# Performance work log

Measured on AMD Instinct MI355X. Metric: run time of the kernel, lower is better.

Reference implementation:

```python
import jax, jax.numpy as jnp
import numpy as np

EPS = 1e-12  # F.normalize eps
WIN_SIZE = 200
WIN_STEP = 30  # eval mode (training uses 10)
N_WIN = 30     # 31 windows from length-1100 axis, last one dropped


def setup_inputs() -> dict:
    key = jax.random.key(0)
    ks = jax.random.split(key, 6)
    dim, K, out_dim = 128, 64, 256
    N, H, W = 8, 16, 900
    s = 1.0 / np.sqrt(dim)
    return {
        "x": jax.random.normal(ks[0], (N, dim, H, W), dtype=jnp.float32),
        "cluster_centers": jax.random.uniform(ks[1], (K, dim), dtype=jnp.float32),
        "conv_w": jax.random.normal(ks[2], (K, dim), dtype=jnp.float32) * s,
        "conv_b": jax.random.normal(ks[3], (K,), dtype=jnp.float32) * s,
        "mlp_w": jax.random.normal(ks[4], (out_dim, K * dim), dtype=jnp.float32) * s,
        "mlp_b": jax.random.normal(ks[5], (out_dim,), dtype=jnp.float32) * s,
    }


def _l2norm(v, axis):
    return v / jnp.clip(jnp.linalg.norm(v, axis=axis, keepdims=True), EPS)


def reference(x, cluster_centers, conv_w, conv_b, mlp_w, mlp_b):
    N, C, H, W = x.shape
    K = conv_w.shape[0]
    # 1x1 conv -> soft assignment, softmax over clusters (dim=1 after view(N,K,HW))
    logits = jnp.einsum('nchw,kc->nkhw', x, conv_w) + conv_b[None, :, None, None]
    a = jax.nn.softmax(logits, axis=1)  # (N,K,H,W)
    # Fused weighted residual sum over H (torch sums dim=-2 of (N,K,C,H,W)):
    # vlad_pre[n,k,c,w] = sum_h a[n,k,h,w]*x[n,c,h,w] - centers[k,c]*sum_h a[n,k,h,w]
    wx = jnp.einsum('nkhw,nchw->nkcw', a, x)               # (N,K,C,W)
    asum = a.sum(axis=2)                                    # (N,K,W)
    res = wx - cluster_centers[None, :, :, None] * asum[:, :, None, :]
    # circular pad along yaw: [800:] ++ all ++ [:100] -> length 1100
    res = jnp.concatenate([res[..., 800:], res, res[..., :100]], axis=-1)
    # sliding-window sum, size 200 step 30, drop last window -> 30 windows
    cs = jnp.cumsum(res, axis=-1)
    cs = jnp.concatenate([jnp.zeros(res.shape[:-1] + (1,), res.dtype), cs], axis=-1)
    starts = jnp.arange(N_WIN) * WIN_STEP
    win = cs[..., starts + WIN_SIZE] - cs[..., starts]      # (N,K,C,30)
    vlad = jnp.transpose(win, (0, 3, 1, 2)).reshape(N * N_WIN, K, C)
    vlad = _l2norm(vlad, axis=2)                            # intra-norm per cluster
    vlad = _l2norm(vlad.reshape(N * N_WIN, K * C), axis=1)  # global norm
    out = vlad @ mlp_w.T + mlp_b
    out = _l2norm(out, axis=1)
    return out.reshape(N, N_WIN, -1)
```

## Files before the change

kernel.cpp:

```cpp
#include <hip/hip_runtime.h>
#include <cstddef>

#define EPSF 1e-12f
#define NCB 90
#define NT 30
#define ODIM 256
#define DDIM 8192

typedef unsigned short u16;
typedef __attribute__((ext_vector_type(8))) short short8;
typedef __attribute__((ext_vector_type(4))) float float4v;

__device__ inline u16 f2bf(float f) {
  union { float f; unsigned u; } v; v.f = f;
  unsigned r = v.u + 0x7FFFu + ((v.u >> 16) & 1u);
  return (u16)(r >> 16);
}
__device__ inline float bf2f(u16 h) {
  union { unsigned u; float f; } v; v.u = ((unsigned)h) << 16;
  return v.f;
}

__global__ __launch_bounds__(256, 2) void k1_assign(
    const float* __restrict__ x,
    const float* __restrict__ conv_w,
    const float* __restrict__ conv_b,
    float* __restrict__ P,
    float* __restrict__ PA)
{
  __shared__ u16 wfh[8192];
  __shared__ u16 wfl[8192];
  __shared__ u16 xtf[4096];
  __shared__ u16 xf[4096];
  __shared__ float As[64 * 33];
  __shared__ u16 afr[2048];
  __shared__ float Mf[32];
  __shared__ float sm4[128];
  __shared__ float pasum[256];

  const int bx = blockIdx.x;
  const int n = bx / NCB, cb = bx - n * NCB;
  const int t = threadIdx.x;
  const int lane = t & 63;
  const int w = t >> 6;

  const float* xn = x + (size_t)n * 1843200 + cb * 10;

#pragma unroll 4
  for (int i = 0; i < 32; ++i) {
    int e = t + 256 * i;
    int k = e >> 7, c = e & 127;
    float wv = conv_w[e];
    u16 h = f2bf(wv);
    float lo = wv - bf2f(h);
    int idx = (((k >> 4) * 4 + (c >> 5)) * 64 + (((c >> 3) & 3) << 4) + (k & 15)) * 8 + (c & 7);
    wfh[idx] = h;
    wfl[idx] = f2bf(lo);
  }

  const int colt = w & 1;
  const int kt0 = w >> 1;
  const float bk0 = conv_b[kt0 * 16 + (lane & 15)];
  const float bk1 = conv_b[(kt0 + 2) * 16 + (lane & 15)];

  float4v pacc[8];
#pragma unroll
  for (int i = 0; i < 8; ++i) pacc[i] = (float4v){0.f, 0.f, 0.f, 0.f};
  float pak = 0.f;

  for (int cc = 0; cc < 5; ++cc) {
    __syncthreads();
#pragma unroll
    for (int s = 0; s < 8; ++s) {
      int e2 = t + 256 * s;
      int c = e2 >> 4, p = e2 & 15;
      int cl = 2 * p;
      int g = cc * 32 + cl;
      int h = g / 10, wi = g - 10 * h;
      float2 val = *(const float2*)(xn + (size_t)c * 14400 + h * 900 + wi);
      u16 h0 = f2bf(val.x), h1 = f2bf(val.y);
      int ip = ((c >> 4) * 64 + ((cl >> 3) << 4) + (c & 15)) * 8 + (cl & 7);
      ushort2 pr; pr.x = h0; pr.y = h1;
      *(ushort2*)&xf[ip] = pr;
      int base_t = (((cl >> 4) * 4 + (c >> 5)) * 64 + (((c >> 3) & 3) << 4)) * 8 + (c & 7);
      xtf[base_t + ((cl & 15) << 3)] = h0;
      xtf[base_t + (((cl + 1) & 15) << 3)] = h1;
    }
    __syncthreads();

    {
      float4v d0 = (float4v){0.f, 0.f, 0.f, 0.f};
      float4v d1 = (float4v){0.f, 0.f, 0.f, 0.f};
#pragma unroll
      for (int cb32 = 0; cb32 < 4; ++cb32) {
        short8 xa = *(short8*)&xtf[((colt * 4 + cb32) * 64 + lane) * 8];
        short8 w0h = *(short8*)&wfh[((kt0 * 4 + cb32) * 64 + lane) * 8];
        short8 w0l = *(short8*)&wfl[((kt0 * 4 + cb32) * 64 + lane) * 8];
        short8 w1h = *(short8*)&wfh[(((kt0 + 2) * 4 + cb32) * 64 + lane) * 8];
        short8 w1l = *(short8*)&wfl[(((kt0 + 2) * 4 + cb32) * 64 + lane) * 8];
        d0 = __builtin_amdgcn_mfma_f32_16x16x32_bf16(xa, w0h, d0, 0, 0, 0);
        d0 = __builtin_amdgcn_mfma_f32_16x16x32_bf16(xa, w0l, d0, 0, 0, 0);
        d1 = __builtin_amdgcn_mfma_f32_16x16x32_bf16(xa, w1h, d1, 0, 0, 0);
        d1 = __builtin_amdgcn_mfma_f32_16x16x32_bf16(xa, w1l, d1, 0, 0, 0);
      }
      int colb = colt * 16 + ((lane >> 4) << 2);
      int kr0 = kt0 * 16 + (lane & 15);
      int kr1 = (kt0 + 2) * 16 + (lane & 15);
#pragma unroll
      for (int r = 0; r < 4; ++r) {
        As[kr0 * 33 + colb + r] = d0[r] + bk0;
        As[kr1 * 33 + colb + r] = d1[r] + bk1;
      }
    }
    __syncthreads();

    if (t < 32) {
      float m = -3.4e38f;
#pragma unroll
      for (int kk = 0; kk < 64; ++kk) m = fmaxf(m, As[kk * 33 + t]);
      Mf[t] = m;
    }
    __syncthreads();
    if (t < 128) {
      int col = t & 31, kg = t >> 5;
      float M = Mf[col], s = 0.f;
#pragma unroll
      for (int ii = 0; ii < 16; ++ii) {
        int a = (kg * 16 + ii) * 33 + col;
        float e = __expf(As[a] - M);
        As[a] = e;
        s += e;
      }
      sm4[kg * 32 + col] = s;
    }
    __syncthreads();

    {
      int k = t & 63, cg = t >> 6;
      union { u16 u[8]; short8 v; } cvt;
      float paks = 0.f;
#pragma unroll
      for (int j = 0; j < 8; ++j) {
        int col = cg * 8 + j;
        float inv = 1.f / (sm4[col] + sm4[32 + col] + sm4[64 + col] + sm4[96 + col]);
        float a = As[k * 33 + col] * inv;
        paks += a;
        cvt.u[j] = f2bf(a);
      }
      pak += paks;
      int dst = ((k >> 4) * 64 + (cg << 4) + (k & 15)) * 8;
      *(short8*)&afr[dst] = cvt.v;
    }
    __syncthreads();

    {
      short8 aa = *(short8*)&afr[(w * 64 + lane) * 8];
#pragma unroll
      for (int ct = 0; ct < 8; ++ct) {
        short8 xb = *(short8*)&xf[(ct * 64 + lane) * 8];
        pacc[ct] = __builtin_amdgcn_mfma_f32_16x16x32_bf16(aa, xb, pacc[ct], 0, 0, 0);
      }
    }
  }

  float* Pp = P + (size_t)(n * NCB + cb) * DDIM;
  {
    int krow = w * 16 + ((lane >> 4) << 2);
    int c0 = lane & 15;
#pragma unroll
    for (int ct = 0; ct < 8; ++ct)
#pragma unroll
      for (int r = 0; r < 4; ++r)
        Pp[(krow + r) * 128 + ct * 16 + c0] = pacc[ct][r];
  }
  pasum[t] = pak;
  __syncthreads();
  if (t < 64)
    PA[(size_t)(n * NCB + cb) * 64 + t] =
        pasum[t] + pasum[64 + t] + pasum[128 + t] + pasum[192 + t];
}

__global__ __launch_bounds__(256) void k2_vlad(
    const float* __restrict__ P, const float* __restrict__ PA,
    const float* __restrict__ centers, float* __restrict__ vlad,
    float* __restrict__ gss)
{
  __shared__ float Ak[16];
  __shared__ float red[4];
  const int b = blockIdx.x;
  const int win = b >> 2, eb = b & 3;
  const int n = win / NT, wt = win - n * NT;
  const int t = threadIdx.x;

  if (t < 64) {
    int kk = t >> 2, ii = t & 3;
    float s = 0.f;
#pragma unroll
    for (int ss = 0; ss < 5; ++ss) {
      int i = ii + 4 * ss;
      int cb = (3 * wt + 80 + i) % 90;
      s += PA[((size_t)n * NCB + cb) * 64 + eb * 16 + kk];
    }
    s += __shfl_xor(s, 1);
    s += __shfl_xor(s, 2);
    if (ii == 0) Ak[kk] = s;
  }
  __syncthreads();

  const int e0 = eb * 2048 + t * 8;
  float v[8];
#pragma unroll
  for (int j = 0; j < 8; ++j) v[j] = 0.f;
#pragma unroll 5
  for (int i = 0; i < 20; ++i) {
    int cb = (3 * wt + 80 + i) % 90;
    const float* Pp = P + ((size_t)n * NCB + cb) * DDIM + e0;
    float4 u0 = *(const float4*)Pp;
    float4 u1 = *(const float4*)(Pp + 4);
    v[0] += u0.x; v[1] += u0.y; v[2] += u0.z; v[3] += u0.w;
    v[4] += u1.x; v[5] += u1.y; v[6] += u1.z; v[7] += u1.w;
  }
  const float A = Ak[t >> 4];
  const float* ce = centers + e0;
  float ss8 = 0.f;
#pragma unroll
  for (int j = 0; j < 8; ++j) {
    float val = v[j] - ce[j] * A;
    v[j] = val;
    ss8 += val * val;
  }
  float ssg = ss8;
  ssg += __shfl_xor(ssg, 1);
  ssg += __shfl_xor(ssg, 2);
  ssg += __shfl_xor(ssg, 4);
  ssg += __shfl_xor(ssg, 8);
  float rn = 1.f / fmaxf(sqrtf(ssg), EPSF);
#pragma unroll
  for (int j = 0; j < 8; ++j) v[j] *= rn;
  float ts = ss8 * rn * rn;
  ts += __shfl_xor(ts, 1);
  ts += __shfl_xor(ts, 2);
  ts += __shfl_xor(ts, 4);
  ts += __shfl_xor(ts, 8);
  ts += __shfl_xor(ts, 16);
  ts += __shfl_xor(ts, 32);
  if ((t & 63) == 0) red[t >> 6] = ts;
  __syncthreads();
  if (t == 0) gss[(size_t)win * 4 + eb] = red[0] + red[1] + red[2] + red[3];

  float* vp = vlad + (size_t)win * DDIM + e0;
  *(float4*)vp = make_float4(v[0], v[1], v[2], v[3]);
  *(float4*)(vp + 4) = make_float4(v[4], v[5], v[6], v[7]);
}

__global__ __launch_bounds__(256) void k3_gemm(
    const float* __restrict__ vlad, const float* __restrict__ gss,
    const float* __restrict__ mlp_w, float* __restrict__ part)
{
  __shared__ float va[16 * 68];
  __shared__ float wbt[64 * 129];
  __shared__ float ga[16];
  const int bx = blockIdx.x;
  const int rt = bx % 15;
  const int hx = bx / 15;
  const int ot = hx & 1, ks = hx >> 1;
  const int t = threadIdx.x;

  if (t < 16) {
    int r = rt * 16 + t;
    float s = gss[r * 4] + gss[r * 4 + 1] + gss[r * 4 + 2] + gss[r * 4 + 3];
    ga[t] = 1.f / fmaxf(sqrtf(s), EPSF);
  }

  const int rr = (t >> 5) << 1;
  const int o0 = t & 31;
  float acc[2][4];
#pragma unroll
  for (int a = 0; a < 2; ++a)
#pragma unroll
    for (int u = 0; u < 4; ++u) acc[a][u] = 0.f;

  const int d0 = ks * 512;
  for (int dc = 0; dc < 512; dc += 64) {
    __syncthreads();
    {
      int r = t >> 4, dq = t & 15;
      float4 u = *(const float4*)(vlad + (size_t)(rt * 16 + r) * DDIM + d0 + dc + 4 * dq);
      float g = ga[r];
      u.x *= g; u.y *= g; u.z *= g; u.w *= g;
      *(float4*)&va[r * 68 + 4 * dq] = u;
    }
#pragma unroll
    for (int s = 0; s < 8; ++s) {
      int f = t + 256 * s;
      int o = f >> 4, dq = f & 15;
      float4 u = *(const float4*)(mlp_w + (size_t)(ot * 128 + o) * DDIM + d0 + dc + 4 * dq);
      wbt[(4 * dq + 0) * 129 + o] = u.x;
      wbt[(4 * dq + 1) * 129 + o] = u.y;
      wbt[(4 * dq + 2) * 129 + o] = u.z;
      wbt[(4 * dq + 3) * 129 + o] = u.w;
    }
    __syncthreads();
#pragma unroll 8
    for (int dd = 0; dd < 64; ++dd) {
      float x0 = va[rr * 68 + dd];
      float x1 = va[(rr + 1) * 68 + dd];
      float y0 = wbt[dd * 129 + o0];
      float y1 = wbt[dd * 129 + o0 + 32];
      float y2 = wbt[dd * 129 + o0 + 64];
      float y3 = wbt[dd * 129 + o0 + 96];
      acc[0][0] += x0 * y0; acc[0][1] += x0 * y1; acc[0][2] += x0 * y2; acc[0][3] += x0 * y3;
      acc[1][0] += x1 * y0; acc[1][1] += x1 * y1; acc[1][2] += x1 * y2; acc[1][3] += x1 * y3;
    }
  }
  float* pp = part + ((size_t)ks * 240 + rt * 16) * ODIM + ot * 128;
#pragma unroll
  for (int a = 0; a < 2; ++a)
#pragma unroll
    for (int u = 0; u < 4; ++u)
      pp[(rr + a) * ODIM + o0 + 32 * u] = acc[a][u];
}

__global__ __launch_bounds__(256) void k4_out(
    const float* __restrict__ part, const float* __restrict__ bias,
    float* __restrict__ out)
{
  __shared__ float red[4];
  const int r = blockIdx.x;
  const int o = threadIdx.x;
  float v = bias[o];
#pragma unroll
  for (int s = 0; s < 16; ++s) v += part[((size_t)s * 240 + r) * ODIM + o];
  float ss = v * v;
  ss += __shfl_xor(ss, 32);
  ss += __shfl_xor(ss, 16);
  ss += __shfl_xor(ss, 8);
  ss += __shfl_xor(ss, 4);
  ss += __shfl_xor(ss, 2);
  ss += __shfl_xor(ss, 1);
  if ((o & 63) == 0) red[o >> 6] = ss;
  __syncthreads();
  float total = red[0] + red[1] + red[2] + red[3];
  out[(size_t)r * ODIM + o] = v / fmaxf(sqrtf(total), EPSF);
}

extern "C" void kernel_launch(void* const* d_in, const int* in_sizes, int n_in,
                              void* d_out, int out_size, void* d_ws, size_t ws_size,
                              hipStream_t stream) {
  const float* x       = (const float*)d_in[0];
  const float* centers = (const float*)d_in[1];
  const float* conv_w  = (const float*)d_in[2];
  const float* conv_b  = (const float*)d_in[3];
  const float* mlp_w   = (const float*)d_in[4];
  const float* mlp_b   = (const float*)d_in[5];
  float* out = (float*)d_out;

  float* ws   = (float*)d_ws;
  float* P    = ws;
  float* PA   = P + (size_t)5898240;
  float* vlad = PA + (size_t)46080;
  float* gss  = vlad + (size_t)1966080;
  float* part = ws;

  k1_assign<<<dim3(8 * NCB), dim3(256), 0, stream>>>(x, conv_w, conv_b, P, PA);
  k2_vlad  <<<dim3(8 * NT * 4), dim3(256), 0, stream>>>(P, PA, centers, vlad, gss);
  k3_gemm  <<<dim3(480), dim3(256), 0, stream>>>(vlad, gss, mlp_w, part);
  k4_out   <<<dim3(240), dim3(256), 0, stream>>>(part, mlp_b, out);
}
```

Measured before the change: 187.1 us.

## Replace window sums with prefix-sum differences and keep conv weights in registers

Adds a cumsum kernel that turns the per-block partial VLAD sums P and PA into in-place running sums along the yaw blocks. The window kernel then reads two or three rows per window instead of twenty, which removes most of its repeated global reads. In k1 the split bf16 hi/lo conv weights now live in registers instead of LDS, and the x tiles get padded LDS layouts to cut bank conflicts; the lower LDS use is paired with a launch bound of 3 blocks. In exchange there is an extra kernel launch and a serial 90-step read-modify-write pass over P, plus more register pressure in k1.

Result: slower. 193.9 us (+3.7%).

```diff
diff --git a/kernel.cpp b/kernel.cpp
--- a/kernel.cpp
+++ b/kernel.cpp
@@ -21,17 +21,15 @@
   return v.f;
 }
 
-__global__ __launch_bounds__(256, 2) void k1_assign(
+__global__ __launch_bounds__(256, 3) void k1_assign(
     const float* __restrict__ x,
     const float* __restrict__ conv_w,
     const float* __restrict__ conv_b,
     float* __restrict__ P,
     float* __restrict__ PA)
 {
-  __shared__ u16 wfh[8192];
-  __shared__ u16 wfl[8192];
-  __shared__ u16 xtf[4096];
-  __shared__ u16 xf[4096];
+  __shared__ u16 xtf[4160];
+  __shared__ u16 xf[5120];
   __shared__ float As[64 * 33];
   __shared__ u16 afr[2048];
   __shared__ float Mf[32];
@@ -46,22 +44,39 @@
 
   const float* xn = x + (size_t)n * 1843200 + cb * 10;
 
-#pragma unroll 4
-  for (int i = 0; i < 32; ++i) {
-    int e = t + 256 * i;
-    int k = e >> 7, c = e & 127;
-    float wv = conv_w[e];
-    u16 h = f2bf(wv);
-    float lo = wv - bf2f(h);
-    int idx = (((k >> 4) * 4 + (c >> 5)) * 64 + (((c >> 3) & 3) << 4) + (k & 15)) * 8 + (c & 7);
-    wfh[idx] = h;
-    wfl[idx] = f2bf(lo);
-  }
-
   const int colt = w & 1;
   const int kt0 = w >> 1;
   const float bk0 = conv_b[kt0 * 16 + (lane & 15)];
   const float bk1 = conv_b[(kt0 + 2) * 16 + (lane & 15)];
+
+  short8 w0h[4], w0l[4], w1h[4], w1l[4];
+  {
+    int kr0 = kt0 * 16 + (lane & 15);
+    int kr1 = kr0 + 32;
+    int cbase = (lane >> 4) << 3;
+#pragma unroll
+    for (int cb32 = 0; cb32 < 4; ++cb32) {
+      const float* wp0 = conv_w + (size_t)kr0 * 128 + cb32 * 32 + cbase;
+      const float* wp1 = conv_w + (size_t)kr1 * 128 + cb32 * 32 + cbase;
+      union { u16 u[8]; short8 v; } hh, ll;
+#pragma unroll
+      for (int j = 0; j < 8; ++j) {
+        float fv = wp0[j];
+        u16 h = f2bf(fv);
+        hh.u[j] = h;
+        ll.u[j] = f2bf(fv - bf2f(h));
+      }
+      w0h[cb32] = hh.v; w0l[cb32] = ll.v;
+#pragma unroll
+      for (int j = 0; j < 8; ++j) {
+        float fv = wp1[j];
+        u16 h = f2bf(fv);
+        hh.u[j] = h;
+        ll.u[j] = f2bf(fv - bf2f(h));
+      }
+      w1h[cb32] = hh.v; w1l[cb32] = ll.v;
+    }
+  }
 
   float4v pacc[8];
 #pragma unroll
@@ -79,12 +94,14 @@
       int h = g / 10, wi = g - 10 * h;
       float2 val = *(const float2*)(xn + (size_t)c * 14400 + h * 900 + wi);
       u16 h0 = f2bf(val.x), h1 = f2bf(val.y);
-      int ip = ((c >> 4) * 64 + ((cl >> 3) << 4) + (c & 15)) * 8 + (cl & 7);
+      int ip = (c >> 4) * 640 + (p >> 2) * 160 + (c & 15) * 8 + (cl & 7);
       ushort2 pr; pr.x = h0; pr.y = h1;
       *(ushort2*)&xf[ip] = pr;
-      int base_t = (((cl >> 4) * 4 + (c >> 5)) * 64 + (((c >> 3) & 3) << 4)) * 8 + (c & 7);
-      xtf[base_t + ((cl & 15) << 3)] = h0;
-      xtf[base_t + (((cl + 1) & 15) << 3)] = h1;
+      int F = (p >> 3) * 4 + (c >> 5);
+      int L = (((c >> 3) & 3) << 4) + (cl & 15);
+      int i0 = F * 520 + L * 8 + (c & 7);
+      xtf[i0] = h0;
+      xtf[i0 + 8] = h1;
     }
     __syncthreads();
 
@@ -93,19 +110,15 @@
       float4v d1 = (float4v){0.f, 0.f, 0.f, 0.f};
 #pragma unroll
       for (int cb32 = 0; cb32 < 4; ++cb32) {
-        short8 xa = *(short8*)&xtf[((colt * 4 + cb32) * 64 + lane) * 8];
-        short8 w0h = *(short8*)&wfh[((kt0 * 4 + cb32) * 64 + lane) * 8];
-        short8 w0l = *(short8*)&wfl[((kt0 * 4 + cb32) * 64 + lane) * 8];
-        short8 w1h = *(short8*)&wfh[(((kt0 + 2) * 4 + cb32) * 64 + lane) * 8];
-        short8 w1l = *(short8*)&wfl[(((kt0 + 2) * 4 + cb32) * 64 + lane) * 8];
-        d0 = __builtin_amdgcn_mfma_f32_16x16x32_bf16(xa, w0h, d0, 0, 0, 0);
-        d0 = __builtin_amdgcn_mfma_f32_16x16x32_bf16(xa, w0l, d0, 0, 0, 0);
-        d1 = __builtin_amdgcn_mfma_f32_16x16x32_bf16(xa, w1h, d1, 0, 0, 0);
-        d1 = __builtin_amdgcn_mfma_f32_16x16x32_bf16(xa, w1l, d1, 0, 0, 0);
+        short8 xa = *(short8*)&xtf[(colt * 4 + cb32) * 520 + lane * 8];
+        d0 = __builtin_amdgcn_mfma_f32_16x16x32_bf16(xa, w0h[cb32], d0, 0, 0, 0);
+        d0 = __builtin_amdgcn_mfma_f32_16x16x32_bf16(xa, w0l[cb32], d0, 0, 0, 0);
+        d1 = __builtin_amdgcn_mfma_f32_16x16x32_bf16(xa, w1h[cb32], d1, 0, 0, 0);
+        d1 = __builtin_amdgcn_mfma_f32_16x16x32_bf16(xa, w1l[cb32], d1, 0, 0, 0);
       }
       int colb = colt * 16 + ((lane >> 4) << 2);
       int kr0 = kt0 * 16 + (lane & 15);
-      int kr1 = (kt0 + 2) * 16 + (lane & 15);
+      int kr1 = kr0 + 32;
 #pragma unroll
       for (int r = 0; r < 4; ++r) {
         As[kr0 * 33 + colb + r] = d0[r] + bk0;
@@ -157,7 +170,7 @@
       short8 aa = *(short8*)&afr[(w * 64 + lane) * 8];
 #pragma unroll
       for (int ct = 0; ct < 8; ++ct) {
-        short8 xb = *(short8*)&xf[(ct * 64 + lane) * 8];
+        short8 xb = *(short8*)&xf[ct * 640 + (lane >> 4) * 160 + (lane & 15) * 8];
         pacc[ct] = __builtin_amdgcn_mfma_f32_16x16x32_bf16(aa, xb, pacc[ct], 0, 0, 0);
       }
     }
@@ -180,7 +193,37 @@
         pasum[t] + pasum[64 + t] + pasum[128 + t] + pasum[192 + t];
 }
 
-__global__ __launch_bounds__(256) void k2_vlad(
+__global__ __launch_bounds__(256) void k2a_cumsum(
+    float* __restrict__ P, float* __restrict__ PA)
+{
+  const int b = blockIdx.x;
+  const int t = threadIdx.x;
+  if (b < 256) {
+    const int n = b >> 5;
+    const int e = ((b & 31) << 8) + t;
+    float* p = P + (size_t)n * NCB * DDIM + e;
+    float acc = 0.f;
+#pragma unroll 6
+    for (int i = 0; i < NCB; ++i) {
+      float v = p[(size_t)i * DDIM];
+      acc += v;
+      p[(size_t)i * DDIM] = acc;
+    }
+  } else {
+    const int idx = ((b - 256) << 8) + t;
+    const int n = idx >> 6, k = idx & 63;
+    float* p = PA + (size_t)n * NCB * 64 + k;
+    float acc = 0.f;
+#pragma unroll 6
+    for (int i = 0; i < NCB; ++i) {
+      float v = p[(size_t)i * 64];
+      acc += v;
+      p[(size_t)i * 64] = acc;
+    }
+  }
+}
+
+__global__ __launch_bounds__(256) void k2b_vlad(
     const float* __restrict__ P, const float* __restrict__ PA,
     const float* __restrict__ centers, float* __restrict__ vlad,
     float* __restrict__ gss)
@@ -192,33 +235,38 @@
   const int n = win / NT, wt = win - n * NT;
   const int t = threadIdx.x;
 
-  if (t < 64) {
-    int kk = t >> 2, ii = t & 3;
-    float s = 0.f;
-#pragma unroll
-    for (int ss = 0; ss < 5; ++ss) {
-      int i = ii + 4 * ss;
-      int cb = (3 * wt + 80 + i) % 90;
-      s += PA[((size_t)n * NCB + cb) * 64 + eb * 16 + kk];
-    }
-    s += __shfl_xor(s, 1);
-    s += __shfl_xor(s, 2);
-    if (ii == 0) Ak[kk] = s;
+  const int a = (3 * wt + 80) % 90;
+  const int bidx = a + 20;
+  const bool wrap = bidx > 90;
+  const int i0 = a - 1;
+  const int i1 = wrap ? 89 : bidx - 1;
+  const int i2 = wrap ? bidx - 91 : 0;
+
+  if (t < 16) {
+    int k = eb * 16 + t;
+    const float* pa = PA + (size_t)n * NCB * 64 + k;
+    float s = pa[(size_t)i1 * 64] - pa[(size_t)i0 * 64];
+    if (wrap) s += pa[(size_t)i2 * 64];
+    Ak[t] = s;
   }
   __syncthreads();
 
   const int e0 = eb * 2048 + t * 8;
+  const float* base = P + (size_t)n * NCB * DDIM + e0;
+  const float* R0 = base + (size_t)i0 * DDIM;
+  const float* R1 = base + (size_t)i1 * DDIM;
+  const float* R2 = base + (size_t)i2 * DDIM;
   float v[8];
-#pragma unroll
-  for (int j = 0; j < 8; ++j) v[j] = 0.f;
-#pragma unroll 5
-  for (int i = 0; i < 20; ++i) {
-    int cb = (3 * wt + 80 + i) % 90;
-    const float* Pp = P + ((size_t)n * NCB + cb) * DDIM + e0;
-    float4 u0 = *(const float4*)Pp;
-    float4 u1 = *(const float4*)(Pp + 4);
-    v[0] += u0.x; v[1] += u0.y; v[2] += u0.z; v[3] += u0.w;
-    v[4] += u1.x; v[5] += u1.y; v[6] += u1.z; v[7] += u1.w;
+  {
+    float4 a0 = *(const float4*)R1, a1 = *(const float4*)(R1 + 4);
+    float4 b0 = *(const float4*)R0, b1 = *(const float4*)(R0 + 4);
+    v[0] = a0.x - b0.x; v[1] = a0.y - b0.y; v[2] = a0.z - b0.z; v[3] = a0.w - b0.w;
+    v[4] = a1.x - b1.x; v[5] = a1.y - b1.y; v[6] = a1.z - b1.z; v[7] = a1.w - b1.w;
+    if (wrap) {
+      float4 c0 = *(const float4*)R2, c1 = *(const float4*)(R2 + 4);
+      v[0] += c0.x; v[1] += c0.y; v[2] += c0.z; v[3] += c0.w;
+      v[4] += c1.x; v[5] += c1.y; v[6] += c1.z; v[7] += c1.w;
+    }
   }
   const float A = Ak[t >> 4];
   const float* ce = centers + e0;
@@ -363,7 +411,8 @@
   float* part = ws;
 
   k1_assign<<<dim3(8 * NCB), dim3(256), 0, stream>>>(x, conv_w, conv_b, P, PA);
-  k2_vlad  <<<dim3(8 * NT * 4), dim3(256), 0, stream>>>(P, PA, centers, vlad, gss);
+  k2a_cumsum<<<dim3(258), dim3(256), 0, stream>>>(P, PA);
+  k2b_vlad <<<dim3(8 * NT * 4), dim3(256), 0, stream>>>(P, PA, centers, vlad, gss);
   k3_gemm  <<<dim3(480), dim3(256), 0, stream>>>(vlad, gss, mlp_w, part);
   k4_out   <<<dim3(240), dim3(256), 0, stream>>>(part, mlp_b, out);
 }
```
